# Kernel optimization log

Measured on AMD Instinct MI355X. Metric: run time of the kernel, lower is better.

Reference implementation:

```python
import jax, jax.numpy as jnp
import numpy as np

# Static DAG configuration (mirrors GraphState): 1 input node + L layers of K nodes.
L = 8          # depth layers (well under t_budget=12)
K = 8          # nodes per layer
D = 128        # node hidden width (node.D)
B = 4096       # batch size
INDEG = 4      # in-edges per non-input node
N = 1 + L * K  # total nodes


def _build_graph():
    """Deterministic static edge lists: srcs[l][k, j] = parent node id (topologically earlier)."""
    rng = np.random.default_rng(0)
    srcs = []
    n_prev = 1  # node 0 is the INPUT node
    for _ in range(L):
        srcs.append(rng.integers(0, n_prev, size=(K, INDEG)))
        n_prev += K
    return srcs


def setup_inputs() -> dict:
    key = jax.random.key(0)
    k1, k2, k3 = jax.random.split(key, 3)
    X = jax.random.normal(k1, (B, D), dtype=jnp.float32)
    # scale ~ sqrt(2/(indeg*D)) to keep relu activations O(1) over 8 layers
    W = jax.random.normal(k2, (N, D, D), dtype=jnp.float32) * 0.06
    b = jax.random.normal(k3, (N, D), dtype=jnp.float32) * 0.01
    return {"X_batch": X, "W_all": W, "bias_all": b}


def reference(X_batch, W_all, bias_all):
    srcs = _build_graph()  # static python/numpy index constants -> jit-friendly
    # INPUT node (id 0): input_dim == D so no zero-padding; V_out = relu(X W^T + b)
    v0 = jax.nn.relu(X_batch @ W_all[0].T + bias_all[0])          # (B, D)
    outs = v0[None]                                               # (n_done, B, D)
    node = 1
    for l in range(L):
        idx = srcs[l]                                             # (K, INDEG) static
        V_in = outs[idx].sum(axis=1)                              # inbox gather-sum -> (K, B, D)
        Wl = W_all[node:node + K]                                 # (K, D, D)
        bl = bias_all[node:node + K]                              # (K, D)
        V_weighted = jnp.einsum('kbd,ked->kbe', V_in, Wl) + bl[:, None, :]
        V_out = jax.nn.relu(V_weighted)                           # apply_primitive(relu)
        outs = jnp.concatenate([outs, V_out], axis=0)
        node += K
    # output nodes = last layer; final = mean over fired output nodes
    return outs[-K:].mean(axis=0)                                 # (B, D)
```

## Files before the change

kernel.cpp:

```cpp
#include <hip/hip_runtime.h>
#include <cstdint>
#include <cstring>

#define BATCH   4096
#define DIM     128
#define NLAYERS 8
#define KNODES  8
#define NDEG    4
#define NNODES  65
#define NODE_ELEMS (BATCH * DIM)
#define ROWS    16
#define SLOTS   37
#define TILE_B  (ROWS * 256)
#define NTHREADS 1024

typedef float    f32x4 __attribute__((ext_vector_type(4)));
typedef short    s16x8 __attribute__((ext_vector_type(8)));
typedef uint32_t u32x4 __attribute__((ext_vector_type(4)));

struct LayerSrcs { int p[KNODES][NDEG]; };

struct Sched {
  uint64_t pinfo[NLAYERS * KNODES];
  int8_t   dst[NLAYERS * KNODES];
  int8_t   root_dst;
};

__device__ __forceinline__ uint32_t f2bf(float f) {
  union { float f; uint32_t i; } x; x.f = f;
  return (x.i + 0x7fffu + ((x.i >> 16) & 1u)) >> 16;
}
__device__ __forceinline__ uint32_t pack2(float a, float b) {
  return f2bf(a) | (f2bf(b) << 16);
}

__global__ __launch_bounds__(256)
void pack_w(const float* __restrict__ W, uint16_t* __restrict__ Wp) {
  int gid  = blockIdx.x * 256 + threadIdx.x;
  int lane = gid & 63;
  int n    = (gid >> 6) & 7;
  int ks   = (gid >> 9) & 3;
  int node = gid >> 11;
  int col  = n * 16 + (lane & 15);
  int k0   = ks * 32 + (lane >> 4) * 8;
  const float* src = W + ((size_t)node * DIM + col) * DIM + k0;
  f32x4 v0 = *(const f32x4*)src;
  f32x4 v1 = *(const f32x4*)(src + 4);
  u32x4 pk;
  pk.x = pack2(v0.x, v0.y); pk.y = pack2(v0.z, v0.w);
  pk.z = pack2(v1.x, v1.y); pk.w = pack2(v1.z, v1.w);
  *(u32x4*)(Wp + (size_t)gid * 8) = pk;
}

__global__ __launch_bounds__(NTHREADS)
void dag_exec(const float* __restrict__ X, const uint16_t* __restrict__ Wp,
              const float* __restrict__ bias, uint16_t* __restrict__ outs,
              float* __restrict__ out, Sched sch)
{
  __shared__ char lds[SLOTS * TILE_B + 2048 * 4];
  float* mb = (float*)(lds + (size_t)SLOTS * TILE_B);

  const int t    = threadIdx.x;
  const int lane = t & 63;
  const int wv   = t >> 6;
  const int lr   = lane & 15;
  const int lg   = lane >> 4;
  const int kn   = wv & 7;
  const int h    = wv >> 3;
  const int row0 = blockIdx.x * ROWS;

  mb[t] = 0.f;
  mb[t + 1024] = 0.f;

  if (wv < 2) {
    const int h2 = wv;
    f32x4 acc[4];
#pragma unroll
    for (int n = 0; n < 4; ++n) acc[n] = (f32x4){0.f, 0.f, 0.f, 0.f};
#pragma unroll
    for (int ks = 0; ks < 4; ++ks) {
      const float* xp = X + (size_t)(row0 + lr) * DIM + ks * 32 + lg * 8;
      f32x4 v0 = *(const f32x4*)xp;
      f32x4 v1 = *(const f32x4*)(xp + 4);
      u32x4 pk;
      pk.x = pack2(v0.x, v0.y); pk.y = pack2(v0.z, v0.w);
      pk.z = pack2(v1.x, v1.y); pk.w = pack2(v1.z, v1.w);
      s16x8 af;
      __builtin_memcpy(&af, &pk, 16);
#pragma unroll
      for (int n = 0; n < 4; ++n) {
        const size_t ci = ((size_t)(0 * 4 + ks) * 8 + h2 * 4 + n);
        s16x8 wf = *(const s16x8*)(Wp + (ci << 9) + lane * 8);
        acc[n] = __builtin_amdgcn_mfma_f32_16x16x32_bf16(af, wf, acc[n], 0, 0, 0);
      }
    }
    char* db = lds + (size_t)sch.root_dst * TILE_B;
#pragma unroll
    for (int n = 0; n < 4; ++n) {
      const int col = (h2 * 4 + n) * 16 + lr;
      const float bv = bias[col];
#pragma unroll
      for (int j = 0; j < 4; ++j) {
        const int row = lg * 4 + j;
        float v = fmaxf(acc[n][j] + bv, 0.f);
        *(uint16_t*)(db + ((row * 256 + col * 2) ^ ((row & 7) << 4))) = (uint16_t)f2bf(v);
      }
    }
  }
  __syncthreads();

  for (int l = 0; l < NLAYERS; ++l) {
    const int idx  = l * KNODES + kn;
    const int node = 1 + idx;
    const int dv   = sch.dst[idx];
    const uint64_t pinfo = sch.pinfo[idx];

    if (dv != -3) {
      f32x4 acc[4];
#pragma unroll
      for (int n = 0; n < 4; ++n) acc[n] = (f32x4){0.f, 0.f, 0.f, 0.f};

#pragma unroll
      for (int ks = 0; ks < 4; ++ks) {
        s16x8 af[NDEG];
#pragma unroll
        for (int p = 0; p < NDEG; ++p) {
          const int e  = (int)((pinfo >> (p * 16)) & 0xffff);
          const int ps = (e & 0xff) - 1;
          if (ps >= 0) {
            af[p] = *(const s16x8*)(lds + (size_t)ps * TILE_B +
                     ((lr * 256 + ks * 64 + lg * 16) ^ ((lr & 7) << 4)));
          } else {
            const int pid = e >> 8;
            af[p] = *(const s16x8*)(outs + (size_t)pid * NODE_ELEMS +
                     (size_t)(row0 + lr) * DIM + ks * 32 + lg * 8);
          }
        }
#pragma unroll
        for (int n = 0; n < 4; ++n) {
          const size_t ci = ((size_t)node * 4 + ks) * 8 + h * 4 + n;
          s16x8 wf = *(const s16x8*)(Wp + (ci << 9) + lane * 8);
#pragma unroll
          for (int p = 0; p < NDEG; ++p)
            acc[n] = __builtin_amdgcn_mfma_f32_16x16x32_bf16(af[p], wf, acc[n], 0, 0, 0);
        }
      }

#pragma unroll
      for (int n = 0; n < 4; ++n) {
        const int col = (h * 4 + n) * 16 + lr;
        const float bv = bias[(size_t)node * DIM + col];
        if (dv >= 0) {
          char* db = lds + (size_t)dv * TILE_B;
#pragma unroll
          for (int j = 0; j < 4; ++j) {
            const int row = lg * 4 + j;
            float v = fmaxf(acc[n][j] + bv, 0.f);
            *(uint16_t*)(db + ((row * 256 + col * 2) ^ ((row & 7) << 4))) = (uint16_t)f2bf(v);
          }
        } else if (dv == -1) {
          uint16_t* gb = outs + (size_t)node * NODE_ELEMS + (size_t)row0 * DIM + col;
#pragma unroll
          for (int j = 0; j < 4; ++j) {
            const int row = lg * 4 + j;
            float v = fmaxf(acc[n][j] + bv, 0.f);
            gb[(size_t)row * DIM] = (uint16_t)f2bf(v);
          }
        } else {
#pragma unroll
          for (int j = 0; j < 4; ++j) {
            const int row = lg * 4 + j;
            float v = fmaxf(acc[n][j] + bv, 0.f);
            atomicAdd(mb + row * DIM + col, v);
          }
        }
      }
    }
    __syncthreads();
  }

  {
    const int r = t >> 7, c = t & 127;
    out[(size_t)(row0 + r) * DIM + c]     = mb[t] * 0.125f;
    out[(size_t)(row0 + 8 + r) * DIM + c] = mb[t + 1024] * 0.125f;
  }
}

namespace nprng {
static inline uint32_t hashmix(uint32_t v, uint32_t& hc) {
  v ^= hc; hc *= 0x931e8875u; v *= hc; v ^= v >> 16; return v;
}
static inline uint32_t mixf(uint32_t x, uint32_t y) {
  uint32_t r = x * 0xca01f9ddu - y * 0x4973f715u;
  r ^= r >> 16;
  return r;
}
struct Pcg {
  unsigned __int128 state, inc;
  bool has32; uint32_t saved;
  void step() {
    const unsigned __int128 MUL =
        ((unsigned __int128)2549297995355413924ULL << 64) | 4865540595714422341ULL;
    state = state * MUL + inc;
  }
  void init_seed0() {
    uint32_t pool[4];
    uint32_t hc = 0x43b0d7e5u;
    for (int i = 0; i < 4; ++i) pool[i] = hashmix(0u, hc);
    for (int s = 0; s < 4; ++s)
      for (int d = 0; d < 4; ++d)
        if (s != d) pool[d] = mixf(pool[d], hashmix(pool[s], hc));
    uint32_t st[8];
    uint32_t hb = 0x8b51f9ddu;
    int cyc = 0;
    for (int i = 0; i < 8; ++i) {
      uint32_t dv = pool[cyc]; cyc = (cyc + 1) & 3;
      dv ^= hb; hb *= 0x58f38dedu; dv *= hb; dv ^= dv >> 16;
      st[i] = dv;
    }
    uint64_t v[4];
    for (int i = 0; i < 4; ++i)
      v[i] = (uint64_t)st[2 * i] | ((uint64_t)st[2 * i + 1] << 32);
    unsigned __int128 s128 = ((unsigned __int128)v[0] << 64) | v[1];
    unsigned __int128 i128 = ((unsigned __int128)v[2] << 64) | v[3];
    state = 0; inc = (i128 << 1) | 1;
    step(); state += s128; step();
    has32 = false; saved = 0;
  }
  uint64_t next64() {
    step();
    uint64_t rot = (uint64_t)(state >> 122);
    uint64_t x = (uint64_t)(state >> 64) ^ (uint64_t)state;
    return rot ? ((x >> rot) | (x << (64 - rot))) : x;
  }
  uint32_t next32() {
    if (has32) { has32 = false; return saved; }
    uint64_t v = next64();
    has32 = true; saved = (uint32_t)(v >> 32);
    return (uint32_t)v;
  }
  uint32_t lemire32(uint32_t rng_incl) {
    uint32_t rng_excl = rng_incl + 1u;
    uint64_t m = (uint64_t)next32() * (uint64_t)rng_excl;
    uint32_t leftover = (uint32_t)m;
    if (leftover < rng_excl) {
      uint32_t threshold = (0xFFFFFFFFu - rng_incl) % rng_excl;
      while (leftover < threshold) {
        m = (uint64_t)next32() * (uint64_t)rng_excl;
        leftover = (uint32_t)m;
      }
    }
    return (uint32_t)(m >> 32);
  }
};
}

extern "C" void kernel_launch(void* const* d_in, const int* in_sizes, int n_in,
                              void* d_out, int out_size, void* d_ws, size_t ws_size,
                              hipStream_t stream) {
  const float* X    = (const float*)d_in[0];
  const float* W    = (const float*)d_in[1];
  const float* bias = (const float*)d_in[2];
  float* out        = (float*)d_out;

  uint16_t* Wp   = (uint16_t*)d_ws;
  uint16_t* outs = (uint16_t*)((char*)d_ws + (size_t)NNODES * DIM * DIM * 2);

  nprng::Pcg rng; rng.init_seed0();
  LayerSrcs srcs[NLAYERS];
  int n_prev = 1;
  for (int l = 0; l < NLAYERS; ++l) {
    for (int k = 0; k < KNODES; ++k)
      for (int j = 0; j < NDEG; ++j)
        srcs[l].p[k][j] = (n_prev == 1) ? 0 : (int)rng.lemire32((uint32_t)(n_prev - 1));
    n_prev += KNODES;
  }

  bool alive[NNODES];
  for (int i = 0; i < NNODES; ++i) alive[i] = false;
  for (int i = NNODES - KNODES; i < NNODES; ++i) alive[i] = true;
  for (int l = NLAYERS - 1; l >= 0; --l)
    for (int k = 0; k < KNODES; ++k)
      if (alive[1 + l * KNODES + k])
        for (int j = 0; j < NDEG; ++j) alive[srcs[l].p[k][j]] = true;

  int last_use[NNODES];
  for (int i = 0; i < NNODES; ++i) last_use[i] = -1;
  for (int l = 0; l < NLAYERS; ++l)
    for (int k = 0; k < KNODES; ++k)
      if (alive[1 + l * KNODES + k])
        for (int j = 0; j < NDEG; ++j) {
          int s = srcs[l].p[k][j];
          if (l > last_use[s]) last_use[s] = l;
        }

  int slot_of[NNODES];
  for (int i = 0; i < NNODES; ++i) slot_of[i] = -1;
  int freeStk[SLOTS], nfree = 0;
  for (int i = SLOTS - 1; i >= 0; --i) freeStk[nfree++] = i;

  Sched sch;
  slot_of[0] = freeStk[--nfree];
  sch.root_dst = (int8_t)slot_of[0];

  for (int l = 0; l < NLAYERS; ++l) {
    for (int k = 0; k < KNODES; ++k) {
      const int node = 1 + l * KNODES + k;
      int dv;
      if (!alive[node])            dv = -3;
      else if (l == NLAYERS - 1)   dv = -2;
      else if (nfree > 0)          dv = slot_of[node] = freeStk[--nfree];
      else                         dv = -1;
      sch.dst[l * KNODES + k] = (int8_t)dv;

      uint64_t w64 = 0;
      for (int j = 0; j < NDEG; ++j) {
        const int src = srcs[l].p[k][j];
        const int enc = ((slot_of[src] + 1) & 0xff) | (src << 8);
        w64 |= (uint64_t)enc << (j * 16);
      }
      sch.pinfo[l * KNODES + k] = w64;
    }
    for (int n = 0; n < NNODES; ++n)
      if (slot_of[n] >= 0 && last_use[n] == l) {
        freeStk[nfree++] = slot_of[n];
        slot_of[n] = -1;
      }
  }

  pack_w<<<dim3(520), dim3(256), 0, stream>>>(W, Wp);
  dag_exec<<<dim3(BATCH / ROWS), dim3(NTHREADS), 0, stream>>>(X, Wp, bias, outs, out, sch);
}
```

Measured before the change: 120.9 us.

## Spread root-node GEMM over eight waves and prefetch layer weights early

```diff
diff --git a/kernel.cpp b/kernel.cpp
--- a/kernel.cpp
+++ b/kernel.cpp
@@ -72,11 +72,12 @@
   mb[t] = 0.f;
   mb[t + 1024] = 0.f;
 
-  if (wv < 2) {
-    const int h2 = wv;
-    f32x4 acc[4];
-#pragma unroll
-    for (int n = 0; n < 4; ++n) acc[n] = (f32x4){0.f, 0.f, 0.f, 0.f};
+  if (wv < 8) {
+    f32x4 acc = (f32x4){0.f, 0.f, 0.f, 0.f};
+    s16x8 wf[4];
+#pragma unroll
+    for (int ks = 0; ks < 4; ++ks)
+      wf[ks] = *(const s16x8*)(Wp + (((size_t)(0 * 4 + ks) * 8 + wv) << 9) + lane * 8);
 #pragma unroll
     for (int ks = 0; ks < 4; ++ks) {
       const float* xp = X + (size_t)(row0 + lr) * DIM + ks * 32 + lg * 8;
@@ -87,24 +88,16 @@
       pk.z = pack2(v1.x, v1.y); pk.w = pack2(v1.z, v1.w);
       s16x8 af;
       __builtin_memcpy(&af, &pk, 16);
-#pragma unroll
-      for (int n = 0; n < 4; ++n) {
-        const size_t ci = ((size_t)(0 * 4 + ks) * 8 + h2 * 4 + n);
-        s16x8 wf = *(const s16x8*)(Wp + (ci << 9) + lane * 8);
-        acc[n] = __builtin_amdgcn_mfma_f32_16x16x32_bf16(af, wf, acc[n], 0, 0, 0);
-      }
+      acc = __builtin_amdgcn_mfma_f32_16x16x32_bf16(af, wf[ks], acc, 0, 0, 0);
     }
     char* db = lds + (size_t)sch.root_dst * TILE_B;
-#pragma unroll
-    for (int n = 0; n < 4; ++n) {
-      const int col = (h2 * 4 + n) * 16 + lr;
-      const float bv = bias[col];
-#pragma unroll
-      for (int j = 0; j < 4; ++j) {
-        const int row = lg * 4 + j;
-        float v = fmaxf(acc[n][j] + bv, 0.f);
-        *(uint16_t*)(db + ((row * 256 + col * 2) ^ ((row & 7) << 4))) = (uint16_t)f2bf(v);
-      }
+    const int col = wv * 16 + lr;
+    const float bv = bias[col];
+#pragma unroll
+    for (int j = 0; j < 4; ++j) {
+      const int row = lg * 4 + j;
+      float v = fmaxf(acc[j] + bv, 0.f);
+      *(uint16_t*)(db + ((row * 256 + col * 2) ^ ((row & 7) << 4))) = (uint16_t)f2bf(v);
     }
   }
   __syncthreads();
@@ -116,6 +109,18 @@
     const uint64_t pinfo = sch.pinfo[idx];
 
     if (dv != -3) {
+      s16x8 wf[4][4];
+#pragma unroll
+      for (int ks = 0; ks < 2; ++ks)
+#pragma unroll
+        for (int n = 0; n < 4; ++n)
+          wf[ks][n] = *(const s16x8*)(Wp +
+              ((((size_t)node * 4 + ks) * 8 + h * 4 + n) << 9) + lane * 8);
+      float bv[4];
+#pragma unroll
+      for (int n = 0; n < 4; ++n)
+        bv[n] = bias[(size_t)node * DIM + (h * 4 + n) * 16 + lr];
+
       f32x4 acc[4];
 #pragma unroll
       for (int n = 0; n < 4; ++n) acc[n] = (f32x4){0.f, 0.f, 0.f, 0.f};
@@ -136,26 +141,30 @@
                      (size_t)(row0 + lr) * DIM + ks * 32 + lg * 8);
           }
         }
-#pragma unroll
-        for (int n = 0; n < 4; ++n) {
-          const size_t ci = ((size_t)node * 4 + ks) * 8 + h * 4 + n;
-          s16x8 wf = *(const s16x8*)(Wp + (ci << 9) + lane * 8);
+        if (ks == 0) {
+#pragma unroll
+          for (int k2 = 2; k2 < 4; ++k2)
+#pragma unroll
+            for (int n = 0; n < 4; ++n)
+              wf[k2][n] = *(const s16x8*)(Wp +
+                  ((((size_t)node * 4 + k2) * 8 + h * 4 + n) << 9) + lane * 8);
+        }
+#pragma unroll
+        for (int n = 0; n < 4; ++n)
 #pragma unroll
           for (int p = 0; p < NDEG; ++p)
-            acc[n] = __builtin_amdgcn_mfma_f32_16x16x32_bf16(af[p], wf, acc[n], 0, 0, 0);
-        }
+            acc[n] = __builtin_amdgcn_mfma_f32_16x16x32_bf16(af[p], wf[ks][n], acc[n], 0, 0, 0);
       }
 
 #pragma unroll
       for (int n = 0; n < 4; ++n) {
         const int col = (h * 4 + n) * 16 + lr;
-        const float bv = bias[(size_t)node * DIM + col];
         if (dv >= 0) {
           char* db = lds + (size_t)dv * TILE_B;
 #pragma unroll
           for (int j = 0; j < 4; ++j) {
             const int row = lg * 4 + j;
-            float v = fmaxf(acc[n][j] + bv, 0.f);
+            float v = fmaxf(acc[n][j] + bv[n], 0.f);
             *(uint16_t*)(db + ((row * 256 + col * 2) ^ ((row & 7) << 4))) = (uint16_t)f2bf(v);
           }
         } else if (dv == -1) {
@@ -163,14 +172,14 @@
 #pragma unroll
           for (int j = 0; j < 4; ++j) {
             const int row = lg * 4 + j;
-            float v = fmaxf(acc[n][j] + bv, 0.f);
+            float v = fmaxf(acc[n][j] + bv[n], 0.f);
             gb[(size_t)row * DIM] = (uint16_t)f2bf(v);
           }
         } else {
 #pragma unroll
           for (int j = 0; j < 4; ++j) {
             const int row = lg * 4 + j;
-            float v = fmaxf(acc[n][j] + bv, 0.f);
+            float v = fmaxf(acc[n][j] + bv[n], 0.f);
             atomicAdd(mb + row * DIM + col, v);
           }
         }
```

New measurement: 127.1 us. 1.05x slower.
